# Optimization experiments

Hardware: AMD Instinct MI355X
Metric: run time of the kernel (lower is better)

Reference implementation:

```python
import jax, jax.numpy as jnp
import numpy as np

SAMPLE_RATE = 32000.0
NUM_APPLICATIONS = 3


def _eq_biquad(x, freq, gain, q, sr):
    """torchaudio.functional.equalizer_biquad: peaking EQ biquad + lfilter.
    x: [B, T] float; freq/gain/q: scalars.
    """
    w0 = 2.0 * jnp.pi * freq / sr
    A = jnp.exp(gain / 40.0 * jnp.log(10.0))  # 10 ** (gain / 40)
    alpha = jnp.sin(w0) / (2.0 * q)
    b0 = 1.0 + alpha * A
    b1 = -2.0 * jnp.cos(w0)
    b2 = 1.0 - alpha * A
    a0 = 1.0 + alpha / A
    a1 = -2.0 * jnp.cos(w0)
    a2 = 1.0 - alpha / A
    # normalize by a0 (as torchaudio biquad -> lfilter does)
    b0, b1, b2 = b0 / a0, b1 / a0, b2 / a0
    a1, a2 = a1 / a0, a2 / a0

    B = x.shape[0]
    z = jnp.zeros((B,), x.dtype)

    def step(carry, xn):
        x1, x2, y1, y2 = carry
        yn = b0 * xn + b1 * x1 + b2 * x2 - a1 * y1 - a2 * y2
        return (xn, x1, yn, y1), yn

    # scan over time axis; carry is per-batch state vectors
    _, y = jax.lax.scan(step, (z, z, z, z), x.T)  # y: [T, B]
    return y.T


def setup_inputs() -> dict:
    key = jax.random.key(0)
    k1, k2, k3, k4 = jax.random.split(key, 4)
    clip = jax.random.normal(k1, (128, 160000), dtype=jnp.float32)
    # draws within the module's f/g/q ranges
    freqs = jax.random.uniform(k2, (NUM_APPLICATIONS,), jnp.float32, 100.0, 6000.0)
    gains = jax.random.uniform(k3, (NUM_APPLICATIONS,), jnp.float32, -8.0, 8.0)
    qs = jax.random.uniform(k4, (NUM_APPLICATIONS,), jnp.float32, 1.0, 9.0)
    return {"clip": clip, "freqs": freqs, "gains": gains, "qs": qs}


def reference(clip, freqs, gains, qs):
    x = clip
    for i in range(NUM_APPLICATIONS):
        x = _eq_biquad(x, freqs[i], gains[i], qs[i], SAMPLE_RATE)
    return x
```

## Files before the change

### kernel.cpp

```cpp
#include <hip/hip_runtime.h>
#include <math.h>

#define SRATE 32000.f
#define NB 128
#define NT 160000
#define CL 50
#define TPB 128
#define NCROW 3200
#define BPR 25
#define NBLK (NB*BPR)
#define SEG 50
#define TILEF (TPB*CL)
#define RECROW (NCROW*8)

#ifndef M_PI
#define M_PI 3.14159265358979323846
#endif

__device__ __forceinline__ void coeffs_f32(
    const float* fr, const float* gn, const float* qs, float* c)
{
  #pragma unroll
  for (int f = 0; f < 3; ++f) {
    float w0 = 2.f * (float)M_PI * fr[f] / SRATE;
    float A  = expf(gn[f] * (2.302585093f / 40.f));
    float al = sinf(w0) / (2.f * qs[f]);
    float cw = cosf(w0);
    float a0 = 1.f + al / A;
    c[f*5+0] = (1.f + al*A) / a0;
    c[f*5+1] = -2.f * cw / a0;
    c[f*5+2] = (1.f - al*A) / a0;
    c[f*5+3] = -2.f * cw / a0;
    c[f*5+4] = (1.f - al/A) / a0;
  }
}

#define STEPR(xn, res) do { \
    float y1 = c[0]*(xn) + c[1]*x1  + c[2]*x2   - c[3]*y1p  - c[4]*y1pp;  \
    float y2 = c[5]*y1  + c[6]*y1p + c[7]*y1pp - c[8]*y2p  - c[9]*y2pp;   \
    float y3 = c[10]*y2 + c[11]*y2p + c[12]*y2pp - c[13]*y3p - c[14]*y3pp;\
    (res) = y3;                                                            \
    x2 = x1; x1 = (xn);                                                    \
    y1pp=y1p; y1p=y1; y2pp=y2p; y2p=y2; y3pp=y3p; y3p=y3;                  \
  } while (0)

__device__ __forceinline__ void stage_half(
    const float* __restrict__ src0, float* dst0, int lane)
{
  const float* src = src0 + lane * 4;
  #pragma unroll
  for (int cc = 0; cc < 12; ++cc) {
    __builtin_amdgcn_global_load_lds(
        (const __attribute__((address_space(1))) void*)(src + cc*256),
        (__attribute__((address_space(3))) void*)(dst0 + cc*256), 16, 0, 0);
  }
  if (lane < 32) {
    __builtin_amdgcn_global_load_lds(
        (const __attribute__((address_space(1))) void*)(src + 12*256),
        (__attribute__((address_space(3))) void*)(dst0 + 12*256), 16, 0, 0);
  }
}


__global__ __launch_bounds__(TPB) void eq_a(
    const float* __restrict__ x, const float* __restrict__ fr,
    const float* __restrict__ gn, const float* __restrict__ qs,
    float* __restrict__ eoT)
{
  __shared__ float lds[TILEF];
  const int tid = threadIdx.x, lane = tid & 63, w = tid >> 6;
  const int t = blockIdx.x, row = t / BPR, bi = t % BPR;
  float c[15];
  coeffs_f32(fr, gn, qs, c);
  const float* base = x + (size_t)row * NT + bi * TILEF;
  stage_half(base + w*3200, &lds[w*3200], lane);
  __syncthreads();
  const int ci = bi * TPB + tid;
  float bx1, bx2;
  if (tid == 0) {
    if (bi == 0) { bx1 = 0.f; bx2 = 0.f; }
    else { bx1 = base[-1]; bx2 = base[-2]; }
  } else {
    bx1 = lds[tid*CL - 1]; bx2 = lds[tid*CL - 2];
  }
  float x1 = bx1, x2 = bx2;
  float y1p=0,y1pp=0,y2p=0,y2pp=0,y3p=0,y3pp=0;
  #pragma unroll
  for (int k = 0; k < CL; ++k) {
    float d_; STEPR(lds[tid*CL + k], d_); (void)d_;
  }
  float* ep = eoT + (size_t)row * RECROW + ((size_t)((ci%50)*64 + ci/50))*8;
  float4 r0; r0.x=y1p; r0.y=y1pp; r0.z=y2p; r0.w=y2pp;
  float4 r1; r1.x=y3p; r1.y=y3pp; r1.z=0.f; r1.w=0.f;
  *(float4*)ep = r0; *(float4*)(ep+4) = r1;
}

__global__ __launch_bounds__(64) void eq_b(
    const float* __restrict__ fr, const float* __restrict__ gn,
    const float* __restrict__ qs, const float* __restrict__ eoT,
    float* __restrict__ sgT)
{
  __shared__ double Mb[36], Rb[36], Tb[36];
  __shared__ float Hs[36], Gs[6*36];
  const int l = threadIdx.x, row = blockIdx.x;
  float c[15];
  coeffs_f32(fr, gn, qs, c);
  if (l < 6) {
    double s0=0,s1=0,s2=0,s3=0,s4=0,s5=0;
    if (l==0) s0=1; else if (l==1) s1=1; else if (l==2) s2=1;
    else if (l==3) s3=1; else if (l==4) s4=1; else s5=1;
    double y1 = -(double)c[3]*s0 - (double)c[4]*s1;
    double y2 = (double)c[5]*y1 + (double)c[6]*s0 + (double)c[7]*s1
              - (double)c[8]*s2 - (double)c[9]*s3;
    double y3 = (double)c[10]*y2 + (double)c[11]*s2 + (double)c[12]*s3
              - (double)c[13]*s4 - (double)c[14]*s5;
    Mb[0*6+l]=y1; Mb[1*6+l]=s0; Mb[2*6+l]=y2; Mb[3*6+l]=s2; Mb[4*6+l]=y3; Mb[5*6+l]=s4;
  }
  if (l < 36) Rb[l] = ((l % 7) == 0) ? 1.0 : 0.0;
  __syncthreads();
  const int i = l / 6, j = l % 6;
  int e = CL;
  while (e) {
    if (e & 1) {
      double acc = 0.0;
      if (l < 36) { for (int k = 0; k < 6; ++k) acc += Rb[i*6+k]*Mb[k*6+j]; Tb[l]=acc; }
      __syncthreads();
      if (l < 36) Rb[l] = Tb[l];
      __syncthreads();
    }
    e >>= 1;
    if (e) {
      double acc = 0.0;
      if (l < 36) { for (int k = 0; k < 6; ++k) acc += Mb[i*6+k]*Mb[k*6+j]; Tb[l]=acc; }
      __syncthreads();
      if (l < 36) Mb[l] = Tb[l];
      __syncthreads();
    }
  }
  if (l < 36) { Hs[l] = (float)Rb[l]; Mb[l] = Rb[l]; }
  __syncthreads();
  if (l < 36) Rb[l] = ((l % 7) == 0) ? 1.0 : 0.0;
  __syncthreads();
  e = SEG;
  while (e) {
    if (e & 1) {
      double acc = 0.0;
      if (l < 36) { for (int k = 0; k < 6; ++k) acc += Rb[i*6+k]*Mb[k*6+j]; Tb[l]=acc; }
      __syncthreads();
      if (l < 36) Rb[l] = Tb[l];
      __syncthreads();
    }
    e >>= 1;
    if (e) {
      double acc = 0.0;
      if (l < 36) { for (int k = 0; k < 6; ++k) acc += Mb[i*6+k]*Mb[k*6+j]; Tb[l]=acc; }
      __syncthreads();
      if (l < 36) Mb[l] = Tb[l];
      __syncthreads();
    }
  }
  if (l < 36) Gs[l] = (float)Rb[l];
  __syncthreads();
  for (int k = 1; k < 6; ++k) {
    double acc = 0.0;
    if (l < 36) { for (int m = 0; m < 6; ++m) acc += Rb[i*6+m]*Rb[m*6+j]; Tb[l]=acc; }
    __syncthreads();
    if (l < 36) Rb[l] = Tb[l];
    __syncthreads();
    if (l < 36) Gs[k*36+l] = (float)Rb[l];
    __syncthreads();
  }

  float H[36];
  #pragma unroll
  for (int q = 0; q < 36; ++q) H[q] = Hs[q];
  const float* rbase = eoT + (size_t)row * RECROW;
  float u[6] = {0,0,0,0,0,0};
  for (int jj = 0; jj < SEG; ++jj) {
    const float* ep = rbase + ((size_t)jj*64 + l)*8;
    float4 r0 = *(const float4*)ep, r1 = *(const float4*)(ep+4);
    float ev[6] = {r0.x,r0.y,r0.z,r0.w,r1.x,r1.y};
    float nu[6];
    #pragma unroll
    for (int q = 0; q < 6; ++q) {
      float a = ev[q];
      #pragma unroll
      for (int m = 0; m < 6; ++m) a += H[q*6+m]*u[m];
      nu[q] = a;
    }
    #pragma unroll
    for (int q = 0; q < 6; ++q) u[q] = nu[q];
  }
  float v6[6];
  #pragma unroll
  for (int q = 0; q < 6; ++q) v6[q] = u[q];
  #pragma unroll
  for (int k = 0; k < 6; ++k) {
    const float* G = Gs + k*36;
    float o[6];
    #pragma unroll
    for (int q = 0; q < 6; ++q) o[q] = __shfl_up(v6[q], 1u << k, 64);
    if (l >= (1 << k)) {
      float nv[6];
      #pragma unroll
      for (int q = 0; q < 6; ++q) {
        float a = v6[q];
        #pragma unroll
        for (int m = 0; m < 6; ++m) a += G[q*6+m]*o[m];
        nv[q] = a;
      }
      #pragma unroll
      for (int q = 0; q < 6; ++q) v6[q] = nv[q];
    }
  }
  float s[6];
  #pragma unroll
  for (int q = 0; q < 6; ++q) s[q] = __shfl_up(v6[q], 1, 64);
  if (l == 0) {
    #pragma unroll
    for (int q = 0; q < 6; ++q) s[q] = 0.f;
  }
  float* wbase = sgT + (size_t)row * RECROW;
  for (int jj = 0; jj < SEG; ++jj) {
    const float* ep = rbase + ((size_t)jj*64 + l)*8;
    float4 r0 = *(const float4*)ep, r1 = *(const float4*)(ep+4);
    float ev[6] = {r0.x,r0.y,r0.z,r0.w,r1.x,r1.y};
    float* wp = wbase + ((size_t)jj*64 + l)*8;
    float4 w0; w0.x=s[0]; w0.y=s[1]; w0.z=s[2]; w0.w=s[3];
    float4 w1; w1.x=s[4]; w1.y=s[5]; w1.z=0.f; w1.w=0.f;
    *(float4*)wp = w0; *(float4*)(wp+4) = w1;
    float ns[6];
    #pragma unroll
    for (int q = 0; q < 6; ++q) {
      float a = ev[q];
      #pragma unroll
      for (int m = 0; m < 6; ++m) a += H[q*6+m]*s[m];
      ns[q] = a;
    }
    #pragma unroll
    for (int q = 0; q < 6; ++q) s[q] = ns[q];
  }
}

__global__ __launch_bounds__(TPB) void eq_c(
    const float* __restrict__ x, const float* __restrict__ fr,
    const float* __restrict__ gn, const float* __restrict__ qs,
    const float* __restrict__ sgT, float* __restrict__ y)
{
  __shared__ float lds[TILEF];
  const int tid = threadIdx.x, lane = tid & 63, w = tid >> 6;
  const int t = blockIdx.x, row = t / BPR, bi = t % BPR;
  float c[15];
  coeffs_f32(fr, gn, qs, c);
  const float* base = x + (size_t)row * NT + bi * TILEF;
  stage_half(base + w*3200, &lds[w*3200], lane);
  __syncthreads();
  const int ci = bi * TPB + tid;
  float bx1, bx2;
  if (tid == 0) {
    if (bi == 0) { bx1 = 0.f; bx2 = 0.f; }
    else { bx1 = base[-1]; bx2 = base[-2]; }
  } else {
    bx1 = lds[tid*CL - 1]; bx2 = lds[tid*CL - 2];
  }
  const float* sp = sgT + (size_t)row * RECROW
                  + ((size_t)((ci%50)*64 + ci/50))*8;
  float4 s0 = *(const float4*)sp, s1 = *(const float4*)(sp+4);
  __syncthreads();
  float x1 = bx1, x2 = bx2;
  float y1p=s0.x, y1pp=s0.y, y2p=s0.z, y2pp=s0.w, y3p=s1.x, y3pp=s1.y;
  float* myrow = &lds[tid * CL];
  #pragma unroll
  for (int k = 0; k < CL; ++k) {
    float o_;
    STEPR(myrow[k], o_);
    myrow[k] = o_;
  }
  __syncthreads();
  float* yg = y + (size_t)row * NT + bi * TILEF;
  const float4* l4 = (const float4*)lds;
  float4* yg4 = (float4*)yg;
  #pragma unroll
  for (int it = 0; it < 12; ++it)
    yg4[it*TPB + tid] = l4[it*TPB + tid];
  if (tid < 64) yg4[1536 + tid] = l4[1536 + tid];
}

extern "C" void kernel_launch(void* const* d_in, const int* in_sizes, int n_in,
                              void* d_out, int out_size, void* d_ws, size_t ws_size,
                              hipStream_t stream) {
  const float* clip = (const float*)d_in[0];
  const float* fr   = (const float*)d_in[1];
  const float* gn   = (const float*)d_in[2];
  const float* qs   = (const float*)d_in[3];
  float* out = (float*)d_out;
  float* eoT = (float*)d_ws;
  float* sgT = eoT + (size_t)NB * RECROW;

  eq_a<<<NBLK, TPB, 0, stream>>>(clip, fr, gn, qs, eoT);
  eq_b<<<NB, 64, 0, stream>>>(fr, gn, qs, eoT, sgT);
  eq_c<<<NBLK, TPB, 0, stream>>>(clip, fr, gn, qs, sgT, out);
}
```

Before: 80.25 us.

## Halve chunk length, double threads, add cross-wave scan in carry kernel

```diff
diff --git a/kernel.cpp b/kernel.cpp
--- a/kernel.cpp
+++ b/kernel.cpp
@@ -4,13 +4,13 @@
 #define SRATE 32000.f
 #define NB 128
 #define NT 160000
-#define CL 50
-#define TPB 128
-#define NCROW 3200
+#define CL 25
+#define TPB 256
+#define TILEF (TPB*CL)
+#define NCROW 6400
 #define BPR 25
 #define NBLK (NB*BPR)
-#define SEG 50
-#define TILEF (TPB*CL)
+#define SEG 25
 #define RECROW (NCROW*8)
 
 #ifndef M_PI
@@ -44,130 +44,125 @@
     y1pp=y1p; y1p=y1; y2pp=y2p; y2p=y2; y3pp=y3p; y3p=y3;                  \
   } while (0)
 
-__device__ __forceinline__ void stage_half(
-    const float* __restrict__ src0, float* dst0, int lane)
-{
-  const float* src = src0 + lane * 4;
-  #pragma unroll
-  for (int cc = 0; cc < 12; ++cc) {
-    __builtin_amdgcn_global_load_lds(
-        (const __attribute__((address_space(1))) void*)(src + cc*256),
-        (__attribute__((address_space(3))) void*)(dst0 + cc*256), 16, 0, 0);
-  }
-  if (lane < 32) {
-    __builtin_amdgcn_global_load_lds(
-        (const __attribute__((address_space(1))) void*)(src + 12*256),
-        (__attribute__((address_space(3))) void*)(dst0 + 12*256), 16, 0, 0);
-  }
-}
-
-
 __global__ __launch_bounds__(TPB) void eq_a(
     const float* __restrict__ x, const float* __restrict__ fr,
     const float* __restrict__ gn, const float* __restrict__ qs,
     float* __restrict__ eoT)
 {
   __shared__ float lds[TILEF];
-  const int tid = threadIdx.x, lane = tid & 63, w = tid >> 6;
-  const int t = blockIdx.x, row = t / BPR, bi = t % BPR;
+  const int tid = threadIdx.x;
+  const int b = blockIdx.x;
+  const int row = b / BPR;
+  const int ci = (b % BPR) * TPB + tid;
   float c[15];
   coeffs_f32(fr, gn, qs, c);
-  const float* base = x + (size_t)row * NT + bi * TILEF;
-  stage_half(base + w*3200, &lds[w*3200], lane);
-  __syncthreads();
-  const int ci = bi * TPB + tid;
-  float bx1, bx2;
+  const float4* xg4 = (const float4*)(x + (size_t)b * TILEF);
+  float4* l4 = (float4*)lds;
+  #pragma unroll
+  for (int it = 0; it < 6; ++it) l4[it*TPB + tid] = xg4[it*TPB + tid];
+  if (tid < 64) l4[1536 + tid] = xg4[1536 + tid];
+  __syncthreads();
+  float x1, x2;
   if (tid == 0) {
-    if (bi == 0) { bx1 = 0.f; bx2 = 0.f; }
-    else { bx1 = base[-1]; bx2 = base[-2]; }
+    if (ci == 0) { x1 = 0.f; x2 = 0.f; }
+    else {
+      float2 h = *(const float2*)(x + (size_t)b * TILEF - 2);
+      x1 = h.y; x2 = h.x;
+    }
   } else {
-    bx1 = lds[tid*CL - 1]; bx2 = lds[tid*CL - 2];
-  }
-  float x1 = bx1, x2 = bx2;
+    x1 = lds[tid*CL - 1]; x2 = lds[tid*CL - 2];
+  }
   float y1p=0,y1pp=0,y2p=0,y2pp=0,y3p=0,y3pp=0;
   #pragma unroll
   for (int k = 0; k < CL; ++k) {
     float d_; STEPR(lds[tid*CL + k], d_); (void)d_;
   }
-  float* ep = eoT + (size_t)row * RECROW + ((size_t)((ci%50)*64 + ci/50))*8;
+  const int plane = ci % 25, slot = ci / 25;
+  float* ep = eoT + (size_t)row * RECROW + ((size_t)(plane*TPB + slot))*8;
   float4 r0; r0.x=y1p; r0.y=y1pp; r0.z=y2p; r0.w=y2pp;
   float4 r1; r1.x=y3p; r1.y=y3pp; r1.z=0.f; r1.w=0.f;
   *(float4*)ep = r0; *(float4*)(ep+4) = r1;
 }
 
-__global__ __launch_bounds__(64) void eq_b(
+__global__ __launch_bounds__(TPB) void eq_b(
     const float* __restrict__ fr, const float* __restrict__ gn,
     const float* __restrict__ qs, const float* __restrict__ eoT,
-    float* __restrict__ sgT)
+    float* __restrict__ sgD)
 {
   __shared__ double Mb[36], Rb[36], Tb[36];
-  __shared__ float Hs[36], Gs[6*36];
-  const int l = threadIdx.x, row = blockIdx.x;
+  __shared__ float Hs[36], Gs[6*36], W64[36];
+  __shared__ float wtot[4][8];
+  const int tid = threadIdx.x, lane = tid & 63, w = tid >> 6;
+  const int row = blockIdx.x;
   float c[15];
   coeffs_f32(fr, gn, qs, c);
-  if (l < 6) {
+  if (tid < 6) {
     double s0=0,s1=0,s2=0,s3=0,s4=0,s5=0;
-    if (l==0) s0=1; else if (l==1) s1=1; else if (l==2) s2=1;
-    else if (l==3) s3=1; else if (l==4) s4=1; else s5=1;
+    if (tid==0) s0=1; else if (tid==1) s1=1; else if (tid==2) s2=1;
+    else if (tid==3) s3=1; else if (tid==4) s4=1; else s5=1;
     double y1 = -(double)c[3]*s0 - (double)c[4]*s1;
     double y2 = (double)c[5]*y1 + (double)c[6]*s0 + (double)c[7]*s1
               - (double)c[8]*s2 - (double)c[9]*s3;
     double y3 = (double)c[10]*y2 + (double)c[11]*s2 + (double)c[12]*s3
               - (double)c[13]*s4 - (double)c[14]*s5;
-    Mb[0*6+l]=y1; Mb[1*6+l]=s0; Mb[2*6+l]=y2; Mb[3*6+l]=s2; Mb[4*6+l]=y3; Mb[5*6+l]=s4;
-  }
-  if (l < 36) Rb[l] = ((l % 7) == 0) ? 1.0 : 0.0;
-  __syncthreads();
-  const int i = l / 6, j = l % 6;
+    Mb[0*6+tid]=y1; Mb[1*6+tid]=s0; Mb[2*6+tid]=y2;
+    Mb[3*6+tid]=s2; Mb[4*6+tid]=y3; Mb[5*6+tid]=s4;
+  }
+  if (tid < 36) Rb[tid] = ((tid % 7) == 0) ? 1.0 : 0.0;
+  __syncthreads();
+  const int i = tid / 6, j = tid % 6;
   int e = CL;
   while (e) {
     if (e & 1) {
       double acc = 0.0;
-      if (l < 36) { for (int k = 0; k < 6; ++k) acc += Rb[i*6+k]*Mb[k*6+j]; Tb[l]=acc; }
-      __syncthreads();
-      if (l < 36) Rb[l] = Tb[l];
+      if (tid < 36) { for (int k = 0; k < 6; ++k) acc += Rb[i*6+k]*Mb[k*6+j]; Tb[tid]=acc; }
+      __syncthreads();
+      if (tid < 36) Rb[tid] = Tb[tid];
       __syncthreads();
     }
     e >>= 1;
     if (e) {
       double acc = 0.0;
-      if (l < 36) { for (int k = 0; k < 6; ++k) acc += Mb[i*6+k]*Mb[k*6+j]; Tb[l]=acc; }
-      __syncthreads();
-      if (l < 36) Mb[l] = Tb[l];
-      __syncthreads();
-    }
-  }
-  if (l < 36) { Hs[l] = (float)Rb[l]; Mb[l] = Rb[l]; }
-  __syncthreads();
-  if (l < 36) Rb[l] = ((l % 7) == 0) ? 1.0 : 0.0;
+      if (tid < 36) { for (int k = 0; k < 6; ++k) acc += Mb[i*6+k]*Mb[k*6+j]; Tb[tid]=acc; }
+      __syncthreads();
+      if (tid < 36) Mb[tid] = Tb[tid];
+      __syncthreads();
+    }
+  }
+  if (tid < 36) { Hs[tid] = (float)Rb[tid]; Mb[tid] = Rb[tid]; }
+  __syncthreads();
+  if (tid < 36) Rb[tid] = ((tid % 7) == 0) ? 1.0 : 0.0;
   __syncthreads();
   e = SEG;
   while (e) {
     if (e & 1) {
       double acc = 0.0;
-      if (l < 36) { for (int k = 0; k < 6; ++k) acc += Rb[i*6+k]*Mb[k*6+j]; Tb[l]=acc; }
-      __syncthreads();
-      if (l < 36) Rb[l] = Tb[l];
+      if (tid < 36) { for (int k = 0; k < 6; ++k) acc += Rb[i*6+k]*Mb[k*6+j]; Tb[tid]=acc; }
+      __syncthreads();
+      if (tid < 36) Rb[tid] = Tb[tid];
       __syncthreads();
     }
     e >>= 1;
     if (e) {
       double acc = 0.0;
-      if (l < 36) { for (int k = 0; k < 6; ++k) acc += Mb[i*6+k]*Mb[k*6+j]; Tb[l]=acc; }
-      __syncthreads();
-      if (l < 36) Mb[l] = Tb[l];
-      __syncthreads();
-    }
-  }
-  if (l < 36) Gs[l] = (float)Rb[l];
-  __syncthreads();
-  for (int k = 1; k < 6; ++k) {
+      if (tid < 36) { for (int k = 0; k < 6; ++k) acc += Mb[i*6+k]*Mb[k*6+j]; Tb[tid]=acc; }
+      __syncthreads();
+      if (tid < 36) Mb[tid] = Tb[tid];
+      __syncthreads();
+    }
+  }
+  if (tid < 36) Gs[tid] = (float)Rb[tid];
+  __syncthreads();
+  for (int k = 1; k <= 6; ++k) {
     double acc = 0.0;
-    if (l < 36) { for (int m = 0; m < 6; ++m) acc += Rb[i*6+m]*Rb[m*6+j]; Tb[l]=acc; }
+    if (tid < 36) { for (int m = 0; m < 6; ++m) acc += Rb[i*6+m]*Rb[m*6+j]; Tb[tid]=acc; }
     __syncthreads();
-    if (l < 36) Rb[l] = Tb[l];
+    if (tid < 36) Rb[tid] = Tb[tid];
     __syncthreads();
-    if (l < 36) Gs[k*36+l] = (float)Rb[l];
+    if (tid < 36) {
+      if (k <= 5) Gs[k*36 + tid] = (float)Rb[tid];
+      else        W64[tid]       = (float)Rb[tid];
+    }
     __syncthreads();
   }
 
@@ -177,7 +172,7 @@
   const float* rbase = eoT + (size_t)row * RECROW;
   float u[6] = {0,0,0,0,0,0};
   for (int jj = 0; jj < SEG; ++jj) {
-    const float* ep = rbase + ((size_t)jj*64 + l)*8;
+    const float* ep = rbase + ((size_t)(jj*TPB + tid))*8;
     float4 r0 = *(const float4*)ep, r1 = *(const float4*)(ep+4);
     float ev[6] = {r0.x,r0.y,r0.z,r0.w,r1.x,r1.y};
     float nu[6];
@@ -200,7 +195,7 @@
     float o[6];
     #pragma unroll
     for (int q = 0; q < 6; ++q) o[q] = __shfl_up(v6[q], 1u << k, 64);
-    if (l >= (1 << k)) {
+    if (lane >= (1 << k)) {
       float nv[6];
       #pragma unroll
       for (int q = 0; q < 6; ++q) {
@@ -213,19 +208,71 @@
       for (int q = 0; q < 6; ++q) v6[q] = nv[q];
     }
   }
+  if (lane == 63) {
+    #pragma unroll
+    for (int q = 0; q < 6; ++q) wtot[w][q] = v6[q];
+  }
+  __syncthreads();
+  float S[6] = {0,0,0,0,0,0};
+  for (int ww = 0; ww < w; ++ww) {
+    float nS[6];
+    #pragma unroll
+    for (int q = 0; q < 6; ++q) {
+      float a = wtot[ww][q];
+      #pragma unroll
+      for (int m = 0; m < 6; ++m) a += W64[q*6+m]*S[m];
+      nS[q] = a;
+    }
+    #pragma unroll
+    for (int q = 0; q < 6; ++q) S[q] = nS[q];
+  }
+  if (lane == 0) {
+    const float* A = Gs;
+    float nu[6];
+    #pragma unroll
+    for (int q = 0; q < 6; ++q) {
+      float a = u[q];
+      #pragma unroll
+      for (int m = 0; m < 6; ++m) a += A[q*6+m]*S[m];
+      nu[q] = a;
+    }
+    #pragma unroll
+    for (int q = 0; q < 6; ++q) u[q] = nu[q];
+  }
+  #pragma unroll
+  for (int q = 0; q < 6; ++q) v6[q] = u[q];
+  #pragma unroll
+  for (int k = 0; k < 6; ++k) {
+    const float* G = Gs + k*36;
+    float o[6];
+    #pragma unroll
+    for (int q = 0; q < 6; ++q) o[q] = __shfl_up(v6[q], 1u << k, 64);
+    if (lane >= (1 << k)) {
+      float nv[6];
+      #pragma unroll
+      for (int q = 0; q < 6; ++q) {
+        float a = v6[q];
+        #pragma unroll
+        for (int m = 0; m < 6; ++m) a += G[q*6+m]*o[m];
+        nv[q] = a;
+      }
+      #pragma unroll
+      for (int q = 0; q < 6; ++q) v6[q] = nv[q];
+    }
+  }
   float s[6];
   #pragma unroll
   for (int q = 0; q < 6; ++q) s[q] = __shfl_up(v6[q], 1, 64);
-  if (l == 0) {
-    #pragma unroll
-    for (int q = 0; q < 6; ++q) s[q] = 0.f;
-  }
-  float* wbase = sgT + (size_t)row * RECROW;
+  if (lane == 0) {
+    #pragma unroll
+    for (int q = 0; q < 6; ++q) s[q] = S[q];
+  }
+  float* wbase = sgD + (size_t)row * RECROW;
   for (int jj = 0; jj < SEG; ++jj) {
-    const float* ep = rbase + ((size_t)jj*64 + l)*8;
+    const float* ep = rbase + ((size_t)(jj*TPB + tid))*8;
     float4 r0 = *(const float4*)ep, r1 = *(const float4*)(ep+4);
     float ev[6] = {r0.x,r0.y,r0.z,r0.w,r1.x,r1.y};
-    float* wp = wbase + ((size_t)jj*64 + l)*8;
+    float* wp = wbase + ((size_t)(tid*SEG + jj))*8;
     float4 w0; w0.x=s[0]; w0.y=s[1]; w0.z=s[2]; w0.w=s[3];
     float4 w1; w1.x=s[4]; w1.y=s[5]; w1.z=0.f; w1.w=0.f;
     *(float4*)wp = w0; *(float4*)(wp+4) = w1;
@@ -245,29 +292,34 @@
 __global__ __launch_bounds__(TPB) void eq_c(
     const float* __restrict__ x, const float* __restrict__ fr,
     const float* __restrict__ gn, const float* __restrict__ qs,
-    const float* __restrict__ sgT, float* __restrict__ y)
+    const float* __restrict__ sgD, float* __restrict__ y)
 {
   __shared__ float lds[TILEF];
-  const int tid = threadIdx.x, lane = tid & 63, w = tid >> 6;
-  const int t = blockIdx.x, row = t / BPR, bi = t % BPR;
+  const int tid = threadIdx.x;
+  const int b = blockIdx.x;
+  const int row = b / BPR;
+  const int ci = (b % BPR) * TPB + tid;
   float c[15];
   coeffs_f32(fr, gn, qs, c);
-  const float* base = x + (size_t)row * NT + bi * TILEF;
-  stage_half(base + w*3200, &lds[w*3200], lane);
-  __syncthreads();
-  const int ci = bi * TPB + tid;
-  float bx1, bx2;
+  const float4* xg4 = (const float4*)(x + (size_t)b * TILEF);
+  float4* l4 = (float4*)lds;
+  #pragma unroll
+  for (int it = 0; it < 6; ++it) l4[it*TPB + tid] = xg4[it*TPB + tid];
+  if (tid < 64) l4[1536 + tid] = xg4[1536 + tid];
+  const float* sp = sgD + (size_t)row * RECROW + (size_t)ci * 8;
+  float4 s0 = *(const float4*)sp, s1 = *(const float4*)(sp+4);
+  __syncthreads();
+  float x1, x2;
   if (tid == 0) {
-    if (bi == 0) { bx1 = 0.f; bx2 = 0.f; }
-    else { bx1 = base[-1]; bx2 = base[-2]; }
+    if (ci == 0) { x1 = 0.f; x2 = 0.f; }
+    else {
+      float2 h = *(const float2*)(x + (size_t)b * TILEF - 2);
+      x1 = h.y; x2 = h.x;
+    }
   } else {
-    bx1 = lds[tid*CL - 1]; bx2 = lds[tid*CL - 2];
-  }
-  const float* sp = sgT + (size_t)row * RECROW
-                  + ((size_t)((ci%50)*64 + ci/50))*8;
-  float4 s0 = *(const float4*)sp, s1 = *(const float4*)(sp+4);
-  __syncthreads();
-  float x1 = bx1, x2 = bx2;
+    x1 = lds[tid*CL - 1]; x2 = lds[tid*CL - 2];
+  }
+  __syncthreads();
   float y1p=s0.x, y1pp=s0.y, y2p=s0.z, y2pp=s0.w, y3p=s1.x, y3pp=s1.y;
   float* myrow = &lds[tid * CL];
   #pragma unroll
@@ -277,12 +329,9 @@
     myrow[k] = o_;
   }
   __syncthreads();
-  float* yg = y + (size_t)row * NT + bi * TILEF;
-  const float4* l4 = (const float4*)lds;
-  float4* yg4 = (float4*)yg;
-  #pragma unroll
-  for (int it = 0; it < 12; ++it)
-    yg4[it*TPB + tid] = l4[it*TPB + tid];
+  float4* yg4 = (float4*)(y + (size_t)b * TILEF);
+  #pragma unroll
+  for (int it = 0; it < 6; ++it) yg4[it*TPB + tid] = l4[it*TPB + tid];
   if (tid < 64) yg4[1536 + tid] = l4[1536 + tid];
 }
 
@@ -295,9 +344,9 @@
   const float* qs   = (const float*)d_in[3];
   float* out = (float*)d_out;
   float* eoT = (float*)d_ws;
-  float* sgT = eoT + (size_t)NB * RECROW;
+  float* sgD = eoT + (size_t)NB * RECROW;
 
   eq_a<<<NBLK, TPB, 0, stream>>>(clip, fr, gn, qs, eoT);
-  eq_b<<<NB, 64, 0, stream>>>(fr, gn, qs, eoT, sgT);
-  eq_c<<<NBLK, TPB, 0, stream>>>(clip, fr, gn, qs, sgT, out);
-}
+  eq_b<<<NB, TPB, 0, stream>>>(fr, gn, qs, eoT, sgD);
+  eq_c<<<NBLK, TPB, 0, stream>>>(clip, fr, gn, qs, sgD, out);
+}
```

Measured after the change: 94.44 us. +17.7%, slower.
